# Performance work log

Measured on AMD Instinct MI355X. Metric: run time of the kernel, lower is better.

The kernel has to match this reference:

```python
import jax, jax.numpy as jnp
import numpy as np

N_NODES = 100000
N_EDGES = 3200000
IN_FEAT = 128
HIDDEN = 128
CLASSES = 32


def gcn_conv(x, edge_index, W, b, n_nodes):
    """PyG GCNConv: linear -> symmetric-normalized scatter-add with self-loops -> +bias."""
    src, dst = edge_index[0], edge_index[1]
    loop = jnp.arange(n_nodes, dtype=edge_index.dtype)
    src = jnp.concatenate([src, loop])
    dst = jnp.concatenate([dst, loop])
    # degree (with self-loops) on destination nodes
    deg = jax.ops.segment_sum(jnp.ones_like(dst, dtype=x.dtype), dst, num_segments=n_nodes)
    dinv = jnp.where(deg > 0, jax.lax.rsqrt(deg), 0.0)
    norm = dinv[src] * dinv[dst]  # [E+N]
    h = x @ W  # [N, out]
    msg = h[src] * norm[:, None]  # gather + scale, [E+N, out]
    out = jax.ops.segment_sum(msg, dst, num_segments=n_nodes)  # scatter-add
    return out + b


def setup_inputs() -> dict:
    key = jax.random.key(0)
    k1, k2, k3, k4 = jax.random.split(key, 4)
    x = jax.random.normal(k1, (N_NODES, IN_FEAT), dtype=jnp.float32)
    edge_index = jax.random.randint(k2, (2, N_EDGES), 0, N_NODES, dtype=jnp.int64)
    W1 = jax.random.normal(k3, (IN_FEAT, HIDDEN), dtype=jnp.float32) / np.sqrt(IN_FEAT)
    b1 = jnp.zeros((HIDDEN,), dtype=jnp.float32)
    W2 = jax.random.normal(k4, (HIDDEN, CLASSES), dtype=jnp.float32) / np.sqrt(HIDDEN)
    b2 = jnp.zeros((CLASSES,), dtype=jnp.float32)
    return {"x": x, "edge_index": edge_index, "W1": W1, "b1": b1, "W2": W2, "b2": b2}


def reference(x, edge_index, W1, b1, W2, b2):
    n = x.shape[0]
    h = gcn_conv(x, edge_index, W1, b1, n)
    h = jax.nn.relu(h)
    # dropout p=0.5 is identity in eval mode
    out = gcn_conv(h, edge_index, W2, b2, n)
    return out
```

## Files before the change

### kernel.cpp

```cpp
#include <hip/hip_runtime.h>

#define N_NODES 100000
#define N_EDGES 3200000
#define F_IN 128
#define F_HID 128
#define F_OUT 32
#define CAP 96

#define NBUCK 391
#define CAPB 8960
#define EPT 32

#define BM 64
#define BK 16
#define XPAD 68

typedef float f32x2 __attribute__((ext_vector_type(2)));

__device__ inline unsigned pack_bf16(float a, float b) {
    unsigned ua = __float_as_uint(a);
    ua = (ua + 0x7fffu + ((ua >> 16) & 1u)) >> 16;
    unsigned ub = __float_as_uint(b);
    ub = (ub + 0x7fffu + ((ub >> 16) & 1u)) >> 16;
    return ua | (ub << 16);
}
__device__ inline float lo16(unsigned u) { return __uint_as_float(u << 16); }
__device__ inline float hi16(unsigned u) { return __uint_as_float(u & 0xffff0000u); }

__global__ __launch_bounds__(256) void k_part(const int* __restrict__ ei,
                                              int* __restrict__ gcur,
                                              unsigned* __restrict__ stage) {
    __shared__ int cnt[NBUCK];
    __shared__ int base[NBUCK];
    int tid = threadIdx.x;
    for (int i = tid; i < NBUCK; i += 256) cnt[i] = 0;
    __syncthreads();

    long e0 = (long)blockIdx.x * (256 * EPT);
#pragma unroll 4
    for (int i = 0; i < EPT; ++i) {
        long e = e0 + i * 256 + tid;
        if (e < N_EDGES) atomicAdd(&cnt[ei[N_EDGES + e] >> 8], 1);
    }
    __syncthreads();
    for (int i = tid; i < NBUCK; i += 256) {
        base[i] = atomicAdd(&gcur[i], cnt[i]);
        cnt[i] = 0;
    }
    __syncthreads();
#pragma unroll 4
    for (int i = 0; i < EPT; ++i) {
        long e = e0 + i * 256 + tid;
        if (e < N_EDGES) {
            int s = ei[e];
            int d = ei[N_EDGES + e];
            int b = d >> 8;
            int pos = base[b] + atomicAdd(&cnt[b], 1);
            if (pos < CAPB)
                stage[(size_t)b * CAPB + pos] = ((unsigned)(d & 255) << 17) | (unsigned)s;
        }
    }
}

__global__ __launch_bounds__(256) void k_csr(const unsigned* __restrict__ stage,
                                             const int* __restrict__ gcur,
                                             int* __restrict__ csr,
                                             int* __restrict__ deg,
                                             float* __restrict__ dinv) {
    __shared__ int cnt[256];
    int b = blockIdx.x;
    int tid = threadIdx.x;
    cnt[tid] = 0;
    __syncthreads();

    int d0 = b << 8;
    int m = gcur[b];
    if (m > CAPB) m = CAPB;
    const unsigned* sp = stage + (size_t)b * CAPB;
    for (int i = tid; i < m; i += 256) {
        unsigned rec = __builtin_nontemporal_load(sp + i);
        int s = (int)(rec & 0x1ffffu);
        int dl = (int)(rec >> 17);
        int pos = atomicAdd(&cnt[dl], 1);
        if (pos < CAP) csr[(size_t)(d0 + dl) * CAP + pos] = s;
    }
    __syncthreads();
    int dd = d0 + tid;
    if (dd < N_NODES) {
        int dg = cnt[tid];
        deg[dd] = dg;
        dinv[dd] = rsqrtf((float)(dg + 1));
    }
}

__global__ __launch_bounds__(256) void k_gemm1(const float* __restrict__ x,
                                               const float* __restrict__ W1,
                                               const float* __restrict__ dinv,
                                               unsigned* __restrict__ g1u) {
    __shared__ float xT[BK][XPAD];
    __shared__ float wt[BK][F_HID];

    int tid = threadIdx.x;
    int m0 = blockIdx.x * BM;

    int rg = tid >> 4;
    int cg = tid & 15;
    int r0 = rg * 4;
    int c0 = cg * 8;

    int lr = tid >> 2;
    int lk = (tid & 3) * 4;
    int gr = m0 + lr;
    int grc = gr < N_NODES ? gr : N_NODES - 1;
    const float* xrow = x + (size_t)grc * F_IN + lk;

    float acc[4][8];
#pragma unroll
    for (int i = 0; i < 4; ++i)
#pragma unroll
        for (int j = 0; j < 8; ++j) acc[i][j] = 0.f;

    for (int k0 = 0; k0 < F_IN; k0 += BK) {
        float4 v = *(const float4*)(xrow + k0);
        const float4* w4 = (const float4*)(W1 + (size_t)k0 * F_HID);
        float4 wv0 = w4[tid];
        float4 wv1 = w4[tid + 256];

        xT[lk + 0][lr] = v.x;
        xT[lk + 1][lr] = v.y;
        xT[lk + 2][lr] = v.z;
        xT[lk + 3][lr] = v.w;
        ((float4*)wt)[tid] = wv0;
        ((float4*)wt)[tid + 256] = wv1;
        __syncthreads();

#pragma unroll
        for (int k = 0; k < BK; ++k) {
            float a[4], b[8];
            *(float4*)a = *(const float4*)&xT[k][r0];
            *(float4*)(b + 0) = *(const float4*)&wt[k][c0];
            *(float4*)(b + 4) = *(const float4*)&wt[k][c0 + 4];
#pragma unroll
            for (int i = 0; i < 4; ++i)
#pragma unroll
                for (int j = 0; j < 8; ++j)
                    acc[i][j] = fmaf(a[i], b[j], acc[i][j]);
        }
        __syncthreads();
    }

#pragma unroll
    for (int i = 0; i < 4; ++i) {
        int n = m0 + r0 + i;
        if (n < N_NODES) {
            float s = dinv[n];
            uint4 o;
            o.x = pack_bf16(acc[i][0] * s, acc[i][1] * s);
            o.y = pack_bf16(acc[i][2] * s, acc[i][3] * s);
            o.z = pack_bf16(acc[i][4] * s, acc[i][5] * s);
            o.w = pack_bf16(acc[i][6] * s, acc[i][7] * s);
            *(uint4*)(g1u + (size_t)n * 64 + (c0 >> 1)) = o;
        }
    }
}

__global__ __launch_bounds__(256) void k_pull1_gemm2(const int* __restrict__ csr,
                                                     const int* __restrict__ deg_i,
                                                     const unsigned* __restrict__ g1u,
                                                     const float* __restrict__ dinv,
                                                     const float* __restrict__ b1,
                                                     const float* __restrict__ W2,
                                                     unsigned* __restrict__ g2u) {
    __shared__ float w2l[F_HID * F_OUT];
    __shared__ float al[4][F_HID];
    {
        const float4* w4 = (const float4*)W2;
        float4* wl4 = (float4*)w2l;
#pragma unroll
        for (int i = 0; i < 4; ++i)
            wl4[threadIdx.x + i * 256] = w4[threadIdx.x + i * 256];
    }
    int lane = threadIdx.x & 63;
    int wv = threadIdx.x >> 6;
    int n = __builtin_amdgcn_readfirstlane(blockIdx.x * 4 + wv);

    int deg = deg_i[n];
    if (deg > CAP) deg = CAP;
    const int* crow = csr + (size_t)n * CAP;
    int sidx0 = (lane < deg) ? __builtin_nontemporal_load(crow + lane) : 0;

    f32x2 ac0, ac1, ac2, ac3, ac4, ac5, ac6, ac7;
    {
        unsigned us = g1u[(size_t)n * 64 + lane];
        ac0 = (f32x2){lo16(us), hi16(us)};
        ac1 = (f32x2){0.f, 0.f};
        ac2 = ac1; ac3 = ac1; ac4 = ac1; ac5 = ac1; ac6 = ac1; ac7 = ac1;
    }

#define GATHER(S, ACC)                                            \
    {                                                             \
        const unsigned* p = g1u + ((size_t)(unsigned)(S) << 6);   \
        unsigned v = p[lane];                                     \
        ACC += (f32x2){lo16(v), hi16(v)};                         \
    }

    int m1 = deg < 64 ? deg : 64;
    int j = 0;
    for (; j + 7 < m1; j += 8) {
        int s0 = __builtin_amdgcn_readlane(sidx0, j);
        int s1 = __builtin_amdgcn_readlane(sidx0, j + 1);
        int s2 = __builtin_amdgcn_readlane(sidx0, j + 2);
        int s3 = __builtin_amdgcn_readlane(sidx0, j + 3);
        int s4 = __builtin_amdgcn_readlane(sidx0, j + 4);
        int s5 = __builtin_amdgcn_readlane(sidx0, j + 5);
        int s6 = __builtin_amdgcn_readlane(sidx0, j + 6);
        int s7 = __builtin_amdgcn_readlane(sidx0, j + 7);
        GATHER(s0, ac0) GATHER(s1, ac1) GATHER(s2, ac2) GATHER(s3, ac3)
        GATHER(s4, ac4) GATHER(s5, ac5) GATHER(s6, ac6) GATHER(s7, ac7)
    }
    for (; j < m1; ++j) {
        int s0 = __builtin_amdgcn_readlane(sidx0, j);
        GATHER(s0, ac0)
    }
    if (deg > 64) {
        int sidx1 = __builtin_nontemporal_load(crow + 64 + (lane & 31));
        int m2 = deg - 64;
        for (j = 0; j < m2; ++j) {
            int s0 = __builtin_amdgcn_readlane(sidx1, j);
            GATHER(s0, ac0)
        }
    }
#undef GATHER

    f32x2 a = ((ac0 + ac1) + (ac2 + ac3)) + ((ac4 + ac5) + (ac6 + ac7));

    float di = dinv[n];
    float2 bb = *(const float2*)(b1 + lane * 2);
    float a0 = fmaxf(fmaf(di, a.x, bb.x), 0.f);
    float a1 = fmaxf(fmaf(di, a.y, bb.y), 0.f);
    *(float2*)(&al[wv][lane * 2]) = make_float2(a0, a1);
    __syncthreads();

    int jj = lane & 31, kh = lane >> 5;
    float sum = 0.f;
#pragma unroll
    for (int kk = 0; kk < 64; ++kk) {
        int k = kh * 64 + kk;
        sum = fmaf(al[wv][k], w2l[k * F_OUT + jj], sum);
    }
    sum += __shfl_xor(sum, 32);
    float sv = sum * di;
    int fl16 = lane & 15;
    float sa = __shfl(sv, fl16 * 2);
    float sb = __shfl(sv, fl16 * 2 + 1);
    if (lane < 16) g2u[(size_t)n * 16 + fl16] = pack_bf16(sa, sb);
}

__global__ __launch_bounds__(256) void k_pull2(const int* __restrict__ csr,
                                               const int* __restrict__ deg_i,
                                               const unsigned* __restrict__ g2u,
                                               const float* __restrict__ dinv,
                                               const float* __restrict__ b2,
                                               float* __restrict__ out) {
    int lane = threadIdx.x & 63;
    int wv = threadIdx.x >> 6;
    int qw = lane >> 4, fl = lane & 15;
    int n = blockIdx.x * 16 + wv * 4 + qw;

    unsigned u0 = g2u[(size_t)n * 16 + fl];
    float a0x = lo16(u0), a0y = hi16(u0);
    float a1x = 0.f, a1y = 0.f, a2x = 0.f, a2y = 0.f, a3x = 0.f, a3y = 0.f;
    int deg = deg_i[n];
    if (deg > CAP) deg = CAP;
    const int* crow = csr + (size_t)n * CAP;
    for (int e0 = 0; e0 < deg; e0 += 16) {
        int rem = deg - e0;
        int m = rem < 16 ? rem : 16;
        int sidx = (fl < m) ? __builtin_nontemporal_load(crow + e0 + fl) : 0;
        int j = 0;
        for (; j + 3 < m; j += 4) {
            int s0 = __shfl(sidx, j, 16);
            int s1 = __shfl(sidx, j + 1, 16);
            int s2 = __shfl(sidx, j + 2, 16);
            int s3 = __shfl(sidx, j + 3, 16);
            unsigned v0 = g2u[(unsigned)s0 * 16u + fl];
            unsigned v1 = g2u[(unsigned)s1 * 16u + fl];
            unsigned v2 = g2u[(unsigned)s2 * 16u + fl];
            unsigned v3 = g2u[(unsigned)s3 * 16u + fl];
            a0x += lo16(v0); a0y += hi16(v0);
            a1x += lo16(v1); a1y += hi16(v1);
            a2x += lo16(v2); a2y += hi16(v2);
            a3x += lo16(v3); a3y += hi16(v3);
        }
        for (; j < m; ++j) {
            int s0 = __shfl(sidx, j, 16);
            unsigned v0 = g2u[(unsigned)s0 * 16u + fl];
            a0x += lo16(v0); a0y += hi16(v0);
        }
    }
    float ax = (a0x + a1x) + (a2x + a3x);
    float ay = (a0y + a1y) + (a2y + a3y);

    float di = dinv[n];
    float2 bb = *(const float2*)(b2 + fl * 2);
    f32x2 o;
    o.x = fmaf(di, ax, bb.x);
    o.y = fmaf(di, ay, bb.y);
    __builtin_nontemporal_store(o, (f32x2*)(out + (size_t)n * F_OUT + fl * 2));
}

extern "C" void kernel_launch(void* const* d_in, const int* in_sizes, int n_in,
                              void* d_out, int out_size, void* d_ws, size_t ws_size,
                              hipStream_t stream) {
    const float* x  = (const float*)d_in[0];
    const int*   ei = (const int*)d_in[1];
    const float* W1 = (const float*)d_in[2];
    const float* b1 = (const float*)d_in[3];
    const float* W2 = (const float*)d_in[4];
    const float* b2 = (const float*)d_in[5];
    float* out = (float*)d_out;

    char* ws = (char*)d_ws;
    int*      deg   = (int*)(ws);
    float*    dinv  = (float*)(ws + 524288);
    int*      gcur  = (int*)(ws + 1048576);
    int*      csr   = (int*)(ws + 1572864);
    unsigned* stage = (unsigned*)(ws + 40000000);
    unsigned* g1u   = (unsigned*)(ws + 54016000);
    unsigned* g2u   = (unsigned*)(ws + 79616000);

    (void)hipMemsetAsync(gcur, 0, 4096, stream);
    k_part<<<(N_EDGES + 256 * EPT - 1) / (256 * EPT), 256, 0, stream>>>(ei, gcur, stage);
    k_csr<<<NBUCK, 256, 0, stream>>>(stage, gcur, csr, deg, dinv);

    k_gemm1<<<(N_NODES + BM - 1) / BM, 256, 0, stream>>>(x, W1, dinv, g1u);

    k_pull1_gemm2<<<N_NODES / 4, 256, 0, stream>>>(csr, deg, g1u, dinv, b1, W2, g2u);
    k_pull2<<<N_NODES / 16, 256, 0, stream>>>(csr, deg, g2u, dinv, b2, out);
}
```

Measured before the change: 295.8 us.

## Enlarge GEMM1 tile and process four nodes per wave in fused pull/GEMM2

The GEMM1 tile grows from 64 to 128 rows, so each thread computes an 8x8 output block and W1 tiles are reused across more rows. The fused layer-1 aggregation plus GEMM2 kernel now has each wave handle four nodes in sequence, storing the activations as bf16 in shared memory. This amortizes the per-block load of W2 into shared memory over 16 nodes instead of 4, and each W2 read from shared memory serves four nodes. The costs are lower gather parallelism per wave (four accumulators instead of eight), more registers, a quarter as many blocks, and extra bf16 rounding of the hidden activations.

```diff
diff --git a/kernel.cpp b/kernel.cpp
--- a/kernel.cpp
+++ b/kernel.cpp
@@ -11,9 +11,8 @@
 #define CAPB 8960
 #define EPT 32
 
-#define BM 64
+#define BM 128
 #define BK 16
-#define XPAD 68
 
 typedef float f32x2 __attribute__((ext_vector_type(2)));
 
@@ -97,7 +96,7 @@
                                                const float* __restrict__ W1,
                                                const float* __restrict__ dinv,
                                                unsigned* __restrict__ g1u) {
-    __shared__ float xT[BK][XPAD];
+    __shared__ float xT[BK][BM + 8];
     __shared__ float wt[BK][F_HID];
 
     int tid = threadIdx.x;
@@ -105,43 +104,45 @@
 
     int rg = tid >> 4;
     int cg = tid & 15;
-    int r0 = rg * 4;
+    int r0 = rg * 8;
     int c0 = cg * 8;
 
-    int lr = tid >> 2;
-    int lk = (tid & 3) * 4;
+    int lr = tid >> 1;
+    int lk = (tid & 1) * 8;
     int gr = m0 + lr;
     int grc = gr < N_NODES ? gr : N_NODES - 1;
     const float* xrow = x + (size_t)grc * F_IN + lk;
 
-    float acc[4][8];
-#pragma unroll
-    for (int i = 0; i < 4; ++i)
+    float acc[8][8];
+#pragma unroll
+    for (int i = 0; i < 8; ++i)
 #pragma unroll
         for (int j = 0; j < 8; ++j) acc[i][j] = 0.f;
 
     for (int k0 = 0; k0 < F_IN; k0 += BK) {
-        float4 v = *(const float4*)(xrow + k0);
+        float4 v0 = *(const float4*)(xrow + k0);
+        float4 v1 = *(const float4*)(xrow + k0 + 4);
         const float4* w4 = (const float4*)(W1 + (size_t)k0 * F_HID);
         float4 wv0 = w4[tid];
         float4 wv1 = w4[tid + 256];
 
-        xT[lk + 0][lr] = v.x;
-        xT[lk + 1][lr] = v.y;
-        xT[lk + 2][lr] = v.z;
-        xT[lk + 3][lr] = v.w;
+        xT[lk + 0][lr] = v0.x; xT[lk + 1][lr] = v0.y;
+        xT[lk + 2][lr] = v0.z; xT[lk + 3][lr] = v0.w;
+        xT[lk + 4][lr] = v1.x; xT[lk + 5][lr] = v1.y;
+        xT[lk + 6][lr] = v1.z; xT[lk + 7][lr] = v1.w;
         ((float4*)wt)[tid] = wv0;
         ((float4*)wt)[tid + 256] = wv1;
         __syncthreads();
 
 #pragma unroll
         for (int k = 0; k < BK; ++k) {
-            float a[4], b[8];
-            *(float4*)a = *(const float4*)&xT[k][r0];
+            float a[8], b[8];
+            *(float4*)(a + 0) = *(const float4*)&xT[k][r0];
+            *(float4*)(a + 4) = *(const float4*)&xT[k][r0 + 4];
             *(float4*)(b + 0) = *(const float4*)&wt[k][c0];
             *(float4*)(b + 4) = *(const float4*)&wt[k][c0 + 4];
 #pragma unroll
-            for (int i = 0; i < 4; ++i)
+            for (int i = 0; i < 8; ++i)
 #pragma unroll
                 for (int j = 0; j < 8; ++j)
                     acc[i][j] = fmaf(a[i], b[j], acc[i][j]);
@@ -150,7 +151,7 @@
     }
 
 #pragma unroll
-    for (int i = 0; i < 4; ++i) {
+    for (int i = 0; i < 8; ++i) {
         int n = m0 + r0 + i;
         if (n < N_NODES) {
             float s = dinv[n];
@@ -172,7 +173,7 @@
                                                      const float* __restrict__ W2,
                                                      unsigned* __restrict__ g2u) {
     __shared__ float w2l[F_HID * F_OUT];
-    __shared__ float al[4][F_HID];
+    __shared__ unsigned alu[16][64];
     {
         const float4* w4 = (const float4*)W2;
         float4* wl4 = (float4*)w2l;
@@ -182,20 +183,11 @@
     }
     int lane = threadIdx.x & 63;
     int wv = threadIdx.x >> 6;
-    int n = __builtin_amdgcn_readfirstlane(blockIdx.x * 4 + wv);
-
-    int deg = deg_i[n];
-    if (deg > CAP) deg = CAP;
-    const int* crow = csr + (size_t)n * CAP;
-    int sidx0 = (lane < deg) ? __builtin_nontemporal_load(crow + lane) : 0;
-
-    f32x2 ac0, ac1, ac2, ac3, ac4, ac5, ac6, ac7;
-    {
-        unsigned us = g1u[(size_t)n * 64 + lane];
-        ac0 = (f32x2){lo16(us), hi16(us)};
-        ac1 = (f32x2){0.f, 0.f};
-        ac2 = ac1; ac3 = ac1; ac4 = ac1; ac5 = ac1; ac6 = ac1; ac7 = ac1;
-    }
+    int nb4 = __builtin_amdgcn_readfirstlane(blockIdx.x * 16 + wv * 4);
+
+    int4 deg4 = *(const int4*)(deg_i + nb4);
+    float4 di4 = *(const float4*)(dinv + nb4);
+    float2 bb = *(const float2*)(b1 + lane * 2);
 
 #define GATHER(S, ACC)                                            \
     {                                                             \
@@ -204,56 +196,81 @@
         ACC += (f32x2){lo16(v), hi16(v)};                         \
     }
 
-    int m1 = deg < 64 ? deg : 64;
-    int j = 0;
-    for (; j + 7 < m1; j += 8) {
-        int s0 = __builtin_amdgcn_readlane(sidx0, j);
-        int s1 = __builtin_amdgcn_readlane(sidx0, j + 1);
-        int s2 = __builtin_amdgcn_readlane(sidx0, j + 2);
-        int s3 = __builtin_amdgcn_readlane(sidx0, j + 3);
-        int s4 = __builtin_amdgcn_readlane(sidx0, j + 4);
-        int s5 = __builtin_amdgcn_readlane(sidx0, j + 5);
-        int s6 = __builtin_amdgcn_readlane(sidx0, j + 6);
-        int s7 = __builtin_amdgcn_readlane(sidx0, j + 7);
-        GATHER(s0, ac0) GATHER(s1, ac1) GATHER(s2, ac2) GATHER(s3, ac3)
-        GATHER(s4, ac4) GATHER(s5, ac5) GATHER(s6, ac6) GATHER(s7, ac7)
-    }
-    for (; j < m1; ++j) {
-        int s0 = __builtin_amdgcn_readlane(sidx0, j);
-        GATHER(s0, ac0)
-    }
-    if (deg > 64) {
-        int sidx1 = __builtin_nontemporal_load(crow + 64 + (lane & 31));
-        int m2 = deg - 64;
-        for (j = 0; j < m2; ++j) {
-            int s0 = __builtin_amdgcn_readlane(sidx1, j);
+#pragma unroll
+    for (int i = 0; i < 4; ++i) {
+        int n = nb4 + i;
+        int deg = ((const int*)&deg4)[i];
+        if (deg > CAP) deg = CAP;
+        const int* crow = csr + (size_t)n * CAP;
+        int sidx0 = (lane < deg) ? __builtin_nontemporal_load(crow + lane) : 0;
+
+        unsigned us = g1u[(size_t)n * 64 + lane];
+        f32x2 ac0 = (f32x2){lo16(us), hi16(us)};
+        f32x2 ac1 = (f32x2){0.f, 0.f}, ac2 = ac1, ac3 = ac1;
+
+        int m1 = deg < 64 ? deg : 64;
+        int j = 0;
+        for (; j + 3 < m1; j += 4) {
+            int s0 = __builtin_amdgcn_readlane(sidx0, j);
+            int s1 = __builtin_amdgcn_readlane(sidx0, j + 1);
+            int s2 = __builtin_amdgcn_readlane(sidx0, j + 2);
+            int s3 = __builtin_amdgcn_readlane(sidx0, j + 3);
+            GATHER(s0, ac0) GATHER(s1, ac1) GATHER(s2, ac2) GATHER(s3, ac3)
+        }
+        for (; j < m1; ++j) {
+            int s0 = __builtin_amdgcn_readlane(sidx0, j);
             GATHER(s0, ac0)
         }
+        if (deg > 64) {
+            int sidx1 = __builtin_nontemporal_load(crow + 64 + (lane & 31));
+            int m2 = deg - 64;
+            for (j = 0; j < m2; ++j) {
+                int s0 = __builtin_amdgcn_readlane(sidx1, j);
+                GATHER(s0, ac0)
+            }
+        }
+        f32x2 a = (ac0 + ac1) + (ac2 + ac3);
+        float di = ((const float*)&di4)[i];
+        float a0 = fmaxf(fmaf(di, a.x, bb.x), 0.f);
+        float a1 = fmaxf(fmaf(di, a.y, bb.y), 0.f);
+        alu[wv * 4 + i][lane] = pack_bf16(a0, a1);
     }
 #undef GATHER
-
-    f32x2 a = ((ac0 + ac1) + (ac2 + ac3)) + ((ac4 + ac5) + (ac6 + ac7));
-
-    float di = dinv[n];
-    float2 bb = *(const float2*)(b1 + lane * 2);
-    float a0 = fmaxf(fmaf(di, a.x, bb.x), 0.f);
-    float a1 = fmaxf(fmaf(di, a.y, bb.y), 0.f);
-    *(float2*)(&al[wv][lane * 2]) = make_float2(a0, a1);
     __syncthreads();
 
     int jj = lane & 31, kh = lane >> 5;
-    float sum = 0.f;
-#pragma unroll
-    for (int kk = 0; kk < 64; ++kk) {
-        int k = kh * 64 + kk;
-        sum = fmaf(al[wv][k], w2l[k * F_OUT + jj], sum);
-    }
-    sum += __shfl_xor(sum, 32);
-    float sv = sum * di;
+    f32x2 s0 = {0.f, 0.f}, s1 = s0, s2 = s0, s3 = s0;
+#pragma unroll 4
+    for (int k2 = 0; k2 < 32; ++k2) {
+        int k = kh * 64 + k2 * 2;
+        f32x2 w = (f32x2){w2l[k * F_OUT + jj], w2l[(k + 1) * F_OUT + jj]};
+        int ki = kh * 32 + k2;
+        unsigned p0 = alu[wv * 4 + 0][ki];
+        unsigned p1 = alu[wv * 4 + 1][ki];
+        unsigned p2 = alu[wv * 4 + 2][ki];
+        unsigned p3 = alu[wv * 4 + 3][ki];
+        s0 += (f32x2){lo16(p0), hi16(p0)} * w;
+        s1 += (f32x2){lo16(p1), hi16(p1)} * w;
+        s2 += (f32x2){lo16(p2), hi16(p2)} * w;
+        s3 += (f32x2){lo16(p3), hi16(p3)} * w;
+    }
+    float r0 = s0.x + s0.y, r1 = s1.x + s1.y, r2 = s2.x + s2.y, r3 = s3.x + s3.y;
+    r0 += __shfl_xor(r0, 32); r1 += __shfl_xor(r1, 32);
+    r2 += __shfl_xor(r2, 32); r3 += __shfl_xor(r3, 32);
+    r0 *= ((const float*)&di4)[0]; r1 *= ((const float*)&di4)[1];
+    r2 *= ((const float*)&di4)[2]; r3 *= ((const float*)&di4)[3];
+
     int fl16 = lane & 15;
-    float sa = __shfl(sv, fl16 * 2);
-    float sb = __shfl(sv, fl16 * 2 + 1);
-    if (lane < 16) g2u[(size_t)n * 16 + fl16] = pack_bf16(sa, sb);
+    float sa0 = __shfl(r0, fl16 * 2), sb0 = __shfl(r0, fl16 * 2 + 1);
+    float sa1 = __shfl(r1, fl16 * 2), sb1 = __shfl(r1, fl16 * 2 + 1);
+    float sa2 = __shfl(r2, fl16 * 2), sb2 = __shfl(r2, fl16 * 2 + 1);
+    float sa3 = __shfl(r3, fl16 * 2), sb3 = __shfl(r3, fl16 * 2 + 1);
+    if (lane < 16) {
+        g2u[(size_t)(nb4 + 0) * 16 + fl16] = pack_bf16(sa0, sb0);
+        g2u[(size_t)(nb4 + 1) * 16 + fl16] = pack_bf16(sa1, sb1);
+        g2u[(size_t)(nb4 + 2) * 16 + fl16] = pack_bf16(sa2, sb2);
+        g2u[(size_t)(nb4 + 3) * 16 + fl16] = pack_bf16(sa3, sb3);
+    }
 }
 
 __global__ __launch_bounds__(256) void k_pull2(const int* __restrict__ csr,
@@ -335,6 +352,6 @@
 
     k_gemm1<<<(N_NODES + BM - 1) / BM, 256, 0, stream>>>(x, W1, dinv, g1u);
 
-    k_pull1_gemm2<<<N_NODES / 4, 256, 0, stream>>>(csr, deg, g1u, dinv, b1, W2, g2u);
+    k_pull1_gemm2<<<N_NODES / 16, 256, 0, stream>>>(csr, deg, g1u, dinv, b1, W2, g2u);
     k_pull2<<<N_NODES / 16, 256, 0, stream>>>(csr, deg, g2u, dinv, b2, out);
 }
```

Measured after the change: 293.9 us, median of 2. No clear change (-0.6%).
